# Performance work log

Measured on AMD Instinct MI355X. Metric: run time of the kernel, lower is better.

Reference implementation:

```python
import math
import jax, jax.numpy as jnp
import numpy as np

N_HEAD = 16

def _rope_sin_cos(pos, head_dim, base=10000.0):
    # matches build_sin_cos(seq_len, dim=head_dim//2): inv = base^(-2i/head_dim)
    inv = jnp.exp(jnp.arange(0, head_dim, 2, dtype=jnp.float32) * (-math.log(base) / head_dim))  # (Dh//2,)
    ang = pos[:, None].astype(jnp.float32) * inv[None, :]  # (T, Dh//2)
    return jnp.sin(ang), jnp.cos(ang)

def _apply_rope(q, k, sin, cos):
    # q, k: (B, T, H, Dh); sin/cos: (T, Dh//2)
    half = q.shape[-1] // 2
    s = sin[None, :, None, :]
    c = cos[None, :, None, :]
    q1, q2 = q[..., :half], q[..., half:]
    k1, k2 = k[..., :half], k[..., half:]
    q_rot = jnp.concatenate([q1 * c - q2 * s, q2 * c + q1 * s], axis=-1)
    k_rot = jnp.concatenate([k1 * c - k2 * s, k2 * c + k1 * s], axis=-1)
    return q_rot, k_rot

def setup_inputs() -> dict:
    key = jax.random.key(0)
    k0, k1, k2 = jax.random.split(key, 3)
    B, T, D = 2, 2048, 2048
    x = jax.random.normal(k0, (B, T, D), dtype=jnp.float32)
    w_qkv = jax.random.normal(k1, (3 * D, D), dtype=jnp.float32) * (D ** -0.5)
    w_proj = jax.random.normal(k2, (D, D), dtype=jnp.float32) * (D ** -0.5)
    return {"x": x, "w_qkv": w_qkv, "w_proj": w_proj, "seq_offset": 0}

def reference(x, w_qkv, w_proj, seq_offset):
    # Single-device (world_size=1) ring attention: one hop, so the online
    # lse-merge is the identity; exact causal flash attention + RoPE.
    B, T, D = x.shape
    H = N_HEAD
    Dh = D // H
    qkv = (x @ w_qkv.T).reshape(B, T, 3, H, Dh)
    q, k, v = qkv[:, :, 0], qkv[:, :, 1], qkv[:, :, 2]  # (B, T, H, Dh)
    pos = seq_offset + jnp.arange(T)
    sin, cos = _rope_sin_cos(pos, Dh)
    q, k = _apply_rope(q, k, sin, cos)
    scale = 1.0 / math.sqrt(Dh)  # flash-attn default softmax_scale
    scores = jnp.einsum('bthd,bshd->bhts', q, k) * scale  # (B, H, T, T)
    causal = jnp.tril(jnp.ones((T, T), dtype=bool))
    scores = jnp.where(causal[None, None], scores, -jnp.inf)
    attn = jax.nn.softmax(scores, axis=-1)
    ctx = jnp.einsum('bhts,bshd->bthd', attn, v)  # (B, T, H, Dh)
    out = ctx.reshape(B, T, D) @ w_proj.T
    return out
```

## Files before the change

### kernel.cpp

```cpp
#include <hip/hip_runtime.h>
#include <math.h>

typedef __bf16 bf16x8 __attribute__((ext_vector_type(8)));
typedef float f32x4 __attribute__((ext_vector_type(4)));
typedef unsigned short u16;
typedef unsigned short u16x4 __attribute__((ext_vector_type(4)));
typedef unsigned short u16x8 __attribute__((ext_vector_type(8)));
typedef unsigned int u32;

#define AS1 __attribute__((address_space(1)))
#define AS3 __attribute__((address_space(3)))

static __device__ __forceinline__ float bf2f(u16 u) {
  union { u32 i; float f; } v; v.i = ((u32)u) << 16; return v.f;
}
static __device__ __forceinline__ u16 f2bf(float f) {
  union { __bf16 b; u16 u; } v; v.b = (__bf16)f; return v.u;
}

__global__ __launch_bounds__(256)
void conv_all(const float* __restrict__ x, const float* __restrict__ wq,
              const float* __restrict__ wp, u16* __restrict__ dst) {
  const int gid = blockIdx.x * 256 + threadIdx.x;
  const float* src;
  int off;
  if (gid < 2097152) { src = x; off = gid; }
  else if (gid < 2097152 + 3145728) { src = wq; off = gid - 2097152; }
  else { src = wp; off = gid - (2097152 + 3145728); }
  const float4 v = ((const float4*)src)[off];
  u16x4 p = {f2bf(v.x), f2bf(v.y), f2bf(v.z), f2bf(v.w)};
  ((u16x4*)dst)[gid] = p;
}

template <bool CF32>
__global__ __launch_bounds__(256, 4)
void gemm_bt(const u16* __restrict__ A, const u16* __restrict__ B,
             void* __restrict__ Cp, int M, int N, int K) {
  __shared__ __align__(16) u16 As[128 * 64];
  __shared__ __align__(16) u16 Bs[128 * 64];
  const int tid = threadIdx.x;
  const int lane = tid & 63;
  const int wid = tid >> 6;
  const int wr = wid >> 1, wc = wid & 1;
  const int l15 = lane & 15, l4 = lane >> 4;
  const int m0 = blockIdx.y * 128, n0 = blockIdx.x * 128;

  int grow[4], gkc[4];
#pragma unroll
  for (int i = 0; i < 4; ++i) {
    const int idx = i * 256 + tid;
    grow[i] = idx >> 3;
    gkc[i] = ((idx & 7) ^ (grow[i] & 7)) * 8;
  }

  const f32x4 fzero = {0.f, 0.f, 0.f, 0.f};
  f32x4 acc[4][4];
#pragma unroll
  for (int i = 0; i < 4; ++i)
#pragma unroll
    for (int j = 0; j < 4; ++j) acc[i][j] = fzero;

  for (int kt = 0; kt < K; kt += 64) {
#pragma unroll
    for (int i = 0; i < 4; ++i) {
      __builtin_amdgcn_global_load_lds(
          (AS1 void*)(A + (size_t)(m0 + grow[i]) * K + kt + gkc[i]),
          (AS3 void*)(As + (size_t)(i * 256 + tid) * 8), 16, 0, 0);
      __builtin_amdgcn_global_load_lds(
          (AS1 void*)(B + (size_t)(n0 + grow[i]) * K + kt + gkc[i]),
          (AS3 void*)(Bs + (size_t)(i * 256 + tid) * 8), 16, 0, 0);
    }
    __syncthreads();
    bf16x8 af[4][2], bfr[4][2];
#pragma unroll
    for (int m = 0; m < 4; ++m) {
      const int ra = wr * 64 + m * 16 + l15;
#pragma unroll
      for (int ks = 0; ks < 2; ++ks)
        af[m][ks] = *(const bf16x8*)&As[ra * 64 + (((ks * 4 + l4) ^ (ra & 7)) << 3)];
    }
#pragma unroll
    for (int n = 0; n < 4; ++n) {
      const int rb = wc * 64 + n * 16 + l15;
#pragma unroll
      for (int ks = 0; ks < 2; ++ks)
        bfr[n][ks] = *(const bf16x8*)&Bs[rb * 64 + (((ks * 4 + l4) ^ (rb & 7)) << 3)];
    }
#pragma unroll
    for (int m = 0; m < 4; ++m)
#pragma unroll
      for (int n = 0; n < 4; ++n) {
        acc[m][n] = __builtin_amdgcn_mfma_f32_16x16x32_bf16(af[m][0], bfr[n][0], acc[m][n], 0, 0, 0);
        acc[m][n] = __builtin_amdgcn_mfma_f32_16x16x32_bf16(af[m][1], bfr[n][1], acc[m][n], 0, 0, 0);
      }
    __syncthreads();
  }

#pragma unroll
  for (int m = 0; m < 4; ++m)
#pragma unroll
    for (int r = 0; r < 4; ++r) {
      const int gm = m0 + wr * 64 + m * 16 + l4 * 4 + r;
      if constexpr (CF32) {
        float* crow = (float*)Cp + (size_t)gm * N + n0 + wc * 64 + l15;
#pragma unroll
        for (int n = 0; n < 4; ++n) crow[n * 16] = acc[m][n][r];
      } else {
        u16* crow = (u16*)Cp + (size_t)gm * N + n0 + wc * 64 + l15;
#pragma unroll
        for (int n = 0; n < 4; ++n) crow[n * 16] = f2bf(acc[m][n][r]);
      }
    }
}

__global__ __launch_bounds__(256)
void rope_kernel(u16* __restrict__ qkv, const int* __restrict__ seq_off) {
  const int idx = blockIdx.x * 256 + threadIdx.x;
  const int d8 = idx & 7;
  const int h = (idx >> 3) & 15;
  const int t = (idx >> 7) & 2047;
  const int b = idx >> 18;
  const int d0 = d8 * 8;
  const float pos = (float)(seq_off[0] + t);
  const size_t base = ((size_t)(b * 2048 + t)) * 6144 + h * 128 + d0;
  const u16x8 qlo = *(const u16x8*)(qkv + base);
  const u16x8 qhi = *(const u16x8*)(qkv + base + 64);
  const u16x8 klo = *(const u16x8*)(qkv + base + 2048);
  const u16x8 khi = *(const u16x8*)(qkv + base + 2048 + 64);
  u16x8 qlo_o, qhi_o, klo_o, khi_o;
#pragma unroll
  for (int j = 0; j < 8; ++j) {
    const float inv = expf((float)(d0 + j) * (-0.14391156509731588f));
    float sv, cv;
    sincosf(pos * inv, &sv, &cv);
    const float q1 = bf2f(qlo[j]), q2 = bf2f(qhi[j]);
    qlo_o[j] = f2bf(q1 * cv - q2 * sv);
    qhi_o[j] = f2bf(q2 * cv + q1 * sv);
    const float k1 = bf2f(klo[j]), k2 = bf2f(khi[j]);
    klo_o[j] = f2bf(k1 * cv - k2 * sv);
    khi_o[j] = f2bf(k2 * cv + k1 * sv);
  }
  *(u16x8*)(qkv + base) = qlo_o;
  *(u16x8*)(qkv + base + 64) = qhi_o;
  *(u16x8*)(qkv + base + 2048) = klo_o;
  *(u16x8*)(qkv + base + 2048 + 64) = khi_o;
}

__global__ __launch_bounds__(256, 2)
void attn_kernel(const u16* __restrict__ qkv, u16* __restrict__ ctx) {
  __shared__ __align__(16) u16 kbuf[2][2][32 * 128];
  __shared__ __align__(16) u16 vbuf[2][2][128 * 32];
  __shared__ __align__(16) u16 Plds[4][2][2][16 * 32];
  const int tid = threadIdx.x, lane = tid & 63, w = tid >> 6;
  const int l15 = lane & 15, l4 = lane >> 4;
  const int lin = blockIdx.x;
  const int xcd = lin & 7;
  const int iw = lin >> 3;
  const int bh = xcd + 8 * (iw & 3);
  const int e = iw >> 2;
  const int qt = (e < 8) ? (15 - e) : (e - 8);
  const int b = bh >> 4, h = bh & 15;
  const u16* Qb = qkv + (size_t)b * 2048 * 6144 + h * 128;
  const u16* Kb = Qb + 2048;
  const u16* Vb = Qb + 4096;

  const int sp = tid & 15;
  const int sB = tid >> 4;
  const int sgp = sB & 1;
  const int swg = (((sp >> 2) ^ (sB & 3)) << 3) + ((sp & 3) << 1);
  const int ks0 = (w * 2 + 0) * 64 + lane;
  const int ks1 = (w * 2 + 1) * 64 + lane;
  const int kr0 = ks0 >> 4, kc0 = (ks0 & 15) ^ (kr0 & 15);
  const int kr1 = ks1 >> 4, kc1 = (ks1 & 15) ^ (kr1 & 15);

  const float scale = 0.08838834764831845f;
  const float M0 = 12.0f;
  const f32x4 fzero = {0.f, 0.f, 0.f, 0.f};

  const int q0w = qt * 128 + w * 32;
  const int nt64 = qt * 2 + 2;

  bf16x8 qf[2][4];
#pragma unroll
  for (int rg = 0; rg < 2; ++rg)
#pragma unroll
    for (int c = 0; c < 4; ++c)
      qf[rg][c] = *(const bf16x8*)(Qb + (size_t)(q0w + rg * 16 + l15) * 6144 + c * 32 + l4 * 8);

  f32x4 o[2][8];
#pragma unroll
  for (int rg = 0; rg < 2; ++rg)
#pragma unroll
    for (int ch = 0; ch < 8; ++ch) o[rg][ch] = fzero;
  float lpart[2][4] = {{0.f, 0.f, 0.f, 0.f}, {0.f, 0.f, 0.f, 0.f}};

#pragma unroll
  for (int hh = 0; hh < 2; ++hh) {
    __builtin_amdgcn_global_load_lds(
        (AS1 void*)(Kb + (size_t)(hh * 32 + kr0) * 6144 + kc0 * 8),
        (AS3 void*)(&kbuf[0][hh][(w * 2 + 0) * 512]), 16, 0, 0);
    __builtin_amdgcn_global_load_lds(
        (AS1 void*)(Kb + (size_t)(hh * 32 + kr1) * 6144 + kc1 * 8),
        (AS3 void*)(&kbuf[0][hh][(w * 2 + 1) * 512]), 16, 0, 0);
    const u16* vp = Vb + (size_t)(hh * 32 + 2 * sp) * 6144 + 8 * sB;
    const u16x8 v0 = *(const u16x8*)vp;
    const u16x8 v1 = *(const u16x8*)(vp + 6144);
#pragma unroll
    for (int e2 = 0; e2 < 8; ++e2) {
      const int s = e2 ^ sgp;
      const int dh = 8 * sB + s;
      *(u32*)&vbuf[0][hh][dh * 32 + swg] = (u32)v0[s] | ((u32)v1[s] << 16);
    }
  }
  __syncthreads();

  for (int t = 0; t < nt64; ++t) {
    const int cur = t & 1, nxtb = cur ^ 1;
    const int kv0 = t * 64;
    const bool has_next = (t + 1 < nt64);
    u16x8 va0, va1, vb0, vb1;
    if (has_next) {
      const u16* vp = Vb + (size_t)(kv0 + 64 + 2 * sp) * 6144 + 8 * sB;
      va0 = *(const u16x8*)vp;
      va1 = *(const u16x8*)(vp + 6144);
      const u16* vp2 = vp + (size_t)32 * 6144;
      vb0 = *(const u16x8*)vp2;
      vb1 = *(const u16x8*)(vp2 + 6144);
    }
    f32x4 sv[2][4];
#pragma unroll
    for (int rg = 0; rg < 2; ++rg)
#pragma unroll
      for (int i = 0; i < 4; ++i) sv[rg][i] = fzero;
#pragma unroll
    for (int hh = 0; hh < 2; ++hh) {
#pragma unroll
      for (int c = 0; c < 4; ++c) {
        const bf16x8 kf = *(const bf16x8*)&kbuf[cur][hh][l15 * 128 + (((c * 4 + l4) ^ l15) << 3)];
        sv[0][hh * 2] = __builtin_amdgcn_mfma_f32_16x16x32_bf16(qf[0][c], kf, sv[0][hh * 2], 0, 0, 0);
        sv[1][hh * 2] = __builtin_amdgcn_mfma_f32_16x16x32_bf16(qf[1][c], kf, sv[1][hh * 2], 0, 0, 0);
      }
#pragma unroll
      for (int c = 0; c < 4; ++c) {
        const bf16x8 kf = *(const bf16x8*)&kbuf[cur][hh][(16 + l15) * 128 + (((c * 4 + l4) ^ l15) << 3)];
        sv[0][hh * 2 + 1] = __builtin_amdgcn_mfma_f32_16x16x32_bf16(qf[0][c], kf, sv[0][hh * 2 + 1], 0, 0, 0);
        sv[1][hh * 2 + 1] = __builtin_amdgcn_mfma_f32_16x16x32_bf16(qf[1][c], kf, sv[1][hh * 2 + 1], 0, 0, 0);
      }
    }
    if (has_next) {
#pragma unroll
      for (int hh = 0; hh < 2; ++hh) {
        __builtin_amdgcn_global_load_lds(
            (AS1 void*)(Kb + (size_t)(kv0 + 64 + hh * 32 + kr0) * 6144 + kc0 * 8),
            (AS3 void*)(&kbuf[nxtb][hh][(w * 2 + 0) * 512]), 16, 0, 0);
        __builtin_amdgcn_global_load_lds(
            (AS1 void*)(Kb + (size_t)(kv0 + 64 + hh * 32 + kr1) * 6144 + kc1 * 8),
            (AS3 void*)(&kbuf[nxtb][hh][(w * 2 + 1) * 512]), 16, 0, 0);
      }
    }
#pragma unroll
    for (int rg = 0; rg < 2; ++rg) {
      const int q0r = q0w + rg * 16;
#pragma unroll
      for (int hh = 0; hh < 2; ++hh) {
        const int kb0 = kv0 + hh * 32;
        if (kb0 + 31 <= q0r) {
#pragma unroll
          for (int r = 0; r < 4; ++r) {
            const float p0 = __expf(fmaf(sv[rg][hh * 2][r], scale, -M0));
            const float p1 = __expf(fmaf(sv[rg][hh * 2 + 1][r], scale, -M0));
            lpart[rg][r] += p0 + p1;
            const int row = l4 * 4 + r;
            const int g0 = ((l15 >> 3) ^ l4) & 3;
            const int g1 = (((l15 >> 3) | 2) ^ l4) & 3;
            Plds[w][rg][hh][row * 32 + g0 * 8 + (l15 & 7)] = f2bf(p0);
            Plds[w][rg][hh][row * 32 + g1 * 8 + (l15 & 7)] = f2bf(p1);
          }
        } else {
#pragma unroll
          for (int r = 0; r < 4; ++r) {
            const int qg = q0r + l4 * 4 + r;
            const float p0 = (kb0 + l15 <= qg) ? __expf(fmaf(sv[rg][hh * 2][r], scale, -M0)) : 0.f;
            const float p1 = (kb0 + 16 + l15 <= qg) ? __expf(fmaf(sv[rg][hh * 2 + 1][r], scale, -M0)) : 0.f;
            lpart[rg][r] += p0 + p1;
            const int row = l4 * 4 + r;
            const int g0 = ((l15 >> 3) ^ l4) & 3;
            const int g1 = (((l15 >> 3) | 2) ^ l4) & 3;
            Plds[w][rg][hh][row * 32 + g0 * 8 + (l15 & 7)] = f2bf(p0);
            Plds[w][rg][hh][row * 32 + g1 * 8 + (l15 & 7)] = f2bf(p1);
          }
        }
      }
    }
    __syncthreads();
    const bf16x8 pa00 = *(const bf16x8*)&Plds[w][0][0][l15 * 32 + ((l4 ^ (l15 >> 2)) << 3)];
    const bf16x8 pa01 = *(const bf16x8*)&Plds[w][0][1][l15 * 32 + ((l4 ^ (l15 >> 2)) << 3)];
    const bf16x8 pa10 = *(const bf16x8*)&Plds[w][1][0][l15 * 32 + ((l4 ^ (l15 >> 2)) << 3)];
    const bf16x8 pa11 = *(const bf16x8*)&Plds[w][1][1][l15 * 32 + ((l4 ^ (l15 >> 2)) << 3)];
#pragma unroll
    for (int ch = 0; ch < 8; ++ch) {
      const int dh = ch * 16 + l15;
      const int g = (l4 ^ ((2 * ch + (l15 >> 3)) & 3)) << 3;
      const bf16x8 vf0 = *(const bf16x8*)&vbuf[cur][0][dh * 32 + g];
      o[0][ch] = __builtin_amdgcn_mfma_f32_16x16x32_bf16(pa00, vf0, o[0][ch], 0, 0, 0);
      o[1][ch] = __builtin_amdgcn_mfma_f32_16x16x32_bf16(pa10, vf0, o[1][ch], 0, 0, 0);
      const bf16x8 vf1 = *(const bf16x8*)&vbuf[cur][1][dh * 32 + g];
      o[0][ch] = __builtin_amdgcn_mfma_f32_16x16x32_bf16(pa01, vf1, o[0][ch], 0, 0, 0);
      o[1][ch] = __builtin_amdgcn_mfma_f32_16x16x32_bf16(pa11, vf1, o[1][ch], 0, 0, 0);
    }
    if (has_next) {
#pragma unroll
      for (int e2 = 0; e2 < 8; ++e2) {
        const int s = e2 ^ sgp;
        const int dh = 8 * sB + s;
        *(u32*)&vbuf[nxtb][0][dh * 32 + swg] = (u32)va0[s] | ((u32)va1[s] << 16);
        *(u32*)&vbuf[nxtb][1][dh * 32 + swg] = (u32)vb0[s] | ((u32)vb1[s] << 16);
      }
    }
  }
#pragma unroll
  for (int rg = 0; rg < 2; ++rg) {
    float invl[4];
#pragma unroll
    for (int r = 0; r < 4; ++r) {
      float l = lpart[rg][r];
      l += __shfl_xor(l, 1);
      l += __shfl_xor(l, 2);
      l += __shfl_xor(l, 4);
      l += __shfl_xor(l, 8);
      invl[r] = 1.0f / l;
    }
#pragma unroll
    for (int ch = 0; ch < 8; ++ch)
#pragma unroll
      for (int r = 0; r < 4; ++r) {
        const int gq = q0w + rg * 16 + l4 * 4 + r;
        ctx[(size_t)(b * 2048 + gq) * 2048 + h * 128 + ch * 16 + l15] =
            f2bf(o[rg][ch][r] * invl[r]);
      }
  }
}

extern "C" void kernel_launch(void* const* d_in, const int* in_sizes, int n_in,
                              void* d_out, int out_size, void* d_ws, size_t ws_size,
                              hipStream_t stream) {
  const float* x     = (const float*)d_in[0];
  const float* wqkv  = (const float*)d_in[1];
  const float* wproj = (const float*)d_in[2];
  const int*   soff  = (const int*)d_in[3];
  float* out = (float*)d_out;

  u16* wsu    = (u16*)d_ws;
  u16* xb     = wsu;
  u16* wqkvb  = xb + 8388608;
  u16* wprojb = wqkvb + 12582912;
  u16* qkv    = wprojb + 4194304;
  u16* ctx    = xb;

  conv_all<<<24576, 256, 0, stream>>>(x, wqkv, wproj, wsu);

  gemm_bt<false><<<dim3(48, 32), 256, 0, stream>>>(xb, wqkvb, qkv, 4096, 6144, 2048);
  rope_kernel<<<2048, 256, 0, stream>>>(qkv, soff);
  attn_kernel<<<512, 256, 0, stream>>>(qkv, ctx);
  gemm_bt<true><<<dim3(16, 32), 256, 0, stream>>>(ctx, wprojb, out, 4096, 2048, 2048);
}
```

Baseline: 248.3 us.

## Pre-transpose V in separate kernel and stream it via async global-to-LDS loads

Adds a vtrans kernel that writes V transposed per (batch, head) into a reused workspace region. The attention kernel then loads V tiles straight into LDS with global_load_lds and an XOR swizzle, replacing the per-thread register loads and scattered 32-bit LDS stores that transposed V inside the loop. The goal is to cut VGPR pressure and LDS store work in the attention loop and make the V prefetch asynchronous. In exchange it adds an extra kernel launch and an extra global read and write pass over V.

```diff
diff --git a/kernel.cpp b/kernel.cpp
--- a/kernel.cpp
+++ b/kernel.cpp
@@ -146,10 +146,39 @@
   *(u16x8*)(qkv + base + 2048 + 64) = khi_o;
 }
 
+__global__ __launch_bounds__(256)
+void vtrans(const u16* __restrict__ qkv, u16* __restrict__ vT) {
+  __shared__ __align__(16) u16 tile[64][72];
+  const int lin = blockIdx.x;
+  const int b = lin >> 10, h = (lin >> 6) & 15;
+  const int dht = (lin >> 5) & 1, tt = lin & 31;
+  const int t0 = tt * 64, dh0 = dht * 64;
+  const int tid = threadIdx.x;
+  const u16* Vb = qkv + (size_t)b * 2048 * 6144 + h * 128 + 4096 + dh0;
+#pragma unroll
+  for (int it = 0; it < 2; ++it) {
+    const int idx = it * 256 + tid;
+    const int i = idx >> 3, c = idx & 7;
+    const u16x8 v = *(const u16x8*)(Vb + (size_t)(t0 + i) * 6144 + c * 8);
+#pragma unroll
+    for (int e = 0; e < 8; ++e) tile[c * 8 + e][i] = v[e];
+  }
+  __syncthreads();
+  u16* dst = vT + ((size_t)(b * 16 + h) * 128 + dh0) * 2048 + t0;
+#pragma unroll
+  for (int it = 0; it < 2; ++it) {
+    const int idx = it * 256 + tid;
+    const int j = idx >> 3, ct = idx & 7;
+    const u16x8 o = *(const u16x8*)&tile[j][ct * 8];
+    *(u16x8*)(dst + (size_t)j * 2048 + ct * 8) = o;
+  }
+}
+
 __global__ __launch_bounds__(256, 2)
-void attn_kernel(const u16* __restrict__ qkv, u16* __restrict__ ctx) {
+void attn_kernel(const u16* __restrict__ qkv, const u16* __restrict__ vT,
+                 u16* __restrict__ ctx) {
   __shared__ __align__(16) u16 kbuf[2][2][32 * 128];
-  __shared__ __align__(16) u16 vbuf[2][2][128 * 32];
+  __shared__ __align__(16) u16 vbuf[2][128 * 64];
   __shared__ __align__(16) u16 Plds[4][2][2][16 * 32];
   const int tid = threadIdx.x, lane = tid & 63, w = tid >> 6;
   const int l15 = lane & 15, l4 = lane >> 4;
@@ -162,16 +191,19 @@
   const int b = bh >> 4, h = bh & 15;
   const u16* Qb = qkv + (size_t)b * 2048 * 6144 + h * 128;
   const u16* Kb = Qb + 2048;
-  const u16* Vb = Qb + 4096;
-
-  const int sp = tid & 15;
-  const int sB = tid >> 4;
-  const int sgp = sB & 1;
-  const int swg = (((sp >> 2) ^ (sB & 3)) << 3) + ((sp & 3) << 1);
+  const u16* vTb = vT + (size_t)bh * 128 * 2048;
+
   const int ks0 = (w * 2 + 0) * 64 + lane;
   const int ks1 = (w * 2 + 1) * 64 + lane;
   const int kr0 = ks0 >> 4, kc0 = (ks0 & 15) ^ (kr0 & 15);
   const int kr1 = ks1 >> 4, kc1 = (ks1 & 15) ^ (kr1 & 15);
+  int vrow[4], vkc[4];
+#pragma unroll
+  for (int i = 0; i < 4; ++i) {
+    const int idx = i * 256 + tid;
+    vrow[i] = idx >> 3;
+    vkc[i] = ((idx & 7) ^ (vrow[i] & 7)) * 8;
+  }
 
   const float scale = 0.08838834764831845f;
   const float M0 = 12.0f;
@@ -202,31 +234,18 @@
     __builtin_amdgcn_global_load_lds(
         (AS1 void*)(Kb + (size_t)(hh * 32 + kr1) * 6144 + kc1 * 8),
         (AS3 void*)(&kbuf[0][hh][(w * 2 + 1) * 512]), 16, 0, 0);
-    const u16* vp = Vb + (size_t)(hh * 32 + 2 * sp) * 6144 + 8 * sB;
-    const u16x8 v0 = *(const u16x8*)vp;
-    const u16x8 v1 = *(const u16x8*)(vp + 6144);
-#pragma unroll
-    for (int e2 = 0; e2 < 8; ++e2) {
-      const int s = e2 ^ sgp;
-      const int dh = 8 * sB + s;
-      *(u32*)&vbuf[0][hh][dh * 32 + swg] = (u32)v0[s] | ((u32)v1[s] << 16);
-    }
-  }
+  }
+#pragma unroll
+  for (int i = 0; i < 4; ++i)
+    __builtin_amdgcn_global_load_lds(
+        (AS1 void*)(vTb + (size_t)vrow[i] * 2048 + vkc[i]),
+        (AS3 void*)(&vbuf[0][(i * 256 + tid) * 8]), 16, 0, 0);
   __syncthreads();
 
   for (int t = 0; t < nt64; ++t) {
     const int cur = t & 1, nxtb = cur ^ 1;
     const int kv0 = t * 64;
     const bool has_next = (t + 1 < nt64);
-    u16x8 va0, va1, vb0, vb1;
-    if (has_next) {
-      const u16* vp = Vb + (size_t)(kv0 + 64 + 2 * sp) * 6144 + 8 * sB;
-      va0 = *(const u16x8*)vp;
-      va1 = *(const u16x8*)(vp + 6144);
-      const u16* vp2 = vp + (size_t)32 * 6144;
-      vb0 = *(const u16x8*)vp2;
-      vb1 = *(const u16x8*)(vp2 + 6144);
-    }
     f32x4 sv[2][4];
 #pragma unroll
     for (int rg = 0; rg < 2; ++rg)
@@ -293,6 +312,13 @@
       }
     }
     __syncthreads();
+    if (has_next) {
+#pragma unroll
+      for (int i = 0; i < 4; ++i)
+        __builtin_amdgcn_global_load_lds(
+            (AS1 void*)(vTb + (size_t)vrow[i] * 2048 + kv0 + 64 + vkc[i]),
+            (AS3 void*)(&vbuf[nxtb][(i * 256 + tid) * 8]), 16, 0, 0);
+    }
     const bf16x8 pa00 = *(const bf16x8*)&Plds[w][0][0][l15 * 32 + ((l4 ^ (l15 >> 2)) << 3)];
     const bf16x8 pa01 = *(const bf16x8*)&Plds[w][0][1][l15 * 32 + ((l4 ^ (l15 >> 2)) << 3)];
     const bf16x8 pa10 = *(const bf16x8*)&Plds[w][1][0][l15 * 32 + ((l4 ^ (l15 >> 2)) << 3)];
@@ -300,22 +326,14 @@
 #pragma unroll
     for (int ch = 0; ch < 8; ++ch) {
       const int dh = ch * 16 + l15;
-      const int g = (l4 ^ ((2 * ch + (l15 >> 3)) & 3)) << 3;
-      const bf16x8 vf0 = *(const bf16x8*)&vbuf[cur][0][dh * 32 + g];
+      const int c0 = ((l4 ^ (l15 & 7)) << 3);
+      const int c1 = (((4 + l4) ^ (l15 & 7)) << 3);
+      const bf16x8 vf0 = *(const bf16x8*)&vbuf[cur][dh * 64 + c0];
       o[0][ch] = __builtin_amdgcn_mfma_f32_16x16x32_bf16(pa00, vf0, o[0][ch], 0, 0, 0);
       o[1][ch] = __builtin_amdgcn_mfma_f32_16x16x32_bf16(pa10, vf0, o[1][ch], 0, 0, 0);
-      const bf16x8 vf1 = *(const bf16x8*)&vbuf[cur][1][dh * 32 + g];
+      const bf16x8 vf1 = *(const bf16x8*)&vbuf[cur][dh * 64 + c1];
       o[0][ch] = __builtin_amdgcn_mfma_f32_16x16x32_bf16(pa01, vf1, o[0][ch], 0, 0, 0);
       o[1][ch] = __builtin_amdgcn_mfma_f32_16x16x32_bf16(pa11, vf1, o[1][ch], 0, 0, 0);
-    }
-    if (has_next) {
-#pragma unroll
-      for (int e2 = 0; e2 < 8; ++e2) {
-        const int s = e2 ^ sgp;
-        const int dh = 8 * sB + s;
-        *(u32*)&vbuf[nxtb][0][dh * 32 + swg] = (u32)va0[s] | ((u32)va1[s] << 16);
-        *(u32*)&vbuf[nxtb][1][dh * 32 + swg] = (u32)vb0[s] | ((u32)vb1[s] << 16);
-      }
     }
   }
 #pragma unroll
@@ -356,11 +374,13 @@
   u16* wprojb = wqkvb + 12582912;
   u16* qkv    = wprojb + 4194304;
   u16* ctx    = xb;
+  u16* vT     = wqkvb;
 
   conv_all<<<24576, 256, 0, stream>>>(x, wqkv, wproj, wsu);
 
   gemm_bt<false><<<dim3(48, 32), 256, 0, stream>>>(xb, wqkvb, qkv, 4096, 6144, 2048);
   rope_kernel<<<2048, 256, 0, stream>>>(qkv, soff);
-  attn_kernel<<<512, 256, 0, stream>>>(qkv, ctx);
+  vtrans<<<2048, 256, 0, stream>>>(qkv, vT);
+  attn_kernel<<<512, 256, 0, stream>>>(qkv, vT, ctx);
   gemm_bt<true><<<dim3(16, 32), 256, 0, stream>>>(ctx, wprojb, out, 4096, 2048, 2048);
 }
```

New measurement: 243.4 us. No clear change (-2.0%).
